# Optimization experiments

Measured on AMD Instinct MI355X. Metric: run time of the kernel, lower is better.

## Reference

```python
import jax, jax.numpy as jnp
import numpy as np

N_TOKENS = 16384  # bs*slen = 4*4096
HIDDEN = 2048
EXPERTS = 8
TOPK = 2
EPS = 1e-20


def setup_inputs() -> dict:
    key = jax.random.key(0)
    k1, k2, k3 = jax.random.split(key, 3)
    x = jax.random.normal(k1, (N_TOKENS, HIDDEN), dtype=jnp.float32)
    W = jax.random.normal(k2, (EXPERTS, HIDDEN), dtype=jnp.float32) * 0.02
    expert_bias = jax.random.normal(k3, (EXPERTS,), dtype=jnp.float32) * 0.01
    return {"x": x, "W": W, "expert_bias": expert_bias}


def reference(x, W, expert_bias):
    # gate: linear without bias -> (N, experts)
    logits = jnp.einsum("nd,ed->ne", x, W)
    scores = jax.nn.sigmoid(logits.astype(jnp.float32))
    # topk on biased scores, but gather unbiased scores
    _, selected_experts_indices = jax.lax.top_k(scores + expert_bias[None, :], TOPK)
    top_scores = jnp.take_along_axis(scores, selected_experts_indices, axis=1)
    # renormalize
    top_scores = top_scores / (top_scores.sum(axis=-1, keepdims=True) + EPS)
    # entropy on detached scores
    d = jax.lax.stop_gradient(top_scores)
    experts_entropy = -(d * jnp.log(d)).sum(axis=-1).mean()
    # histogram over expert indices (torch.histc with bins=E, min=0, max=E)
    num_tokens_per_expert = jnp.bincount(
        selected_experts_indices.reshape(-1), length=EXPERTS
    )
    return (top_scores, scores, selected_experts_indices,
            num_tokens_per_expert, experts_entropy)
```

## Files before the change

### kernel.cpp

```cpp
#include <hip/hip_runtime.h>
#include <math.h>

#define NT  16384
#define HID 2048
#define NE  8
#define NBLK 512

constexpr int TOP_OFF  = 0;
constexpr int SC_OFF   = NT * 2;
constexpr int IDX_OFF  = SC_OFF + NT * NE;
constexpr int HIST_OFF = IDX_OFF + NT * 2;
constexpr int ENT_OFF  = HIST_OFF + NE;

constexpr int WS_ROW = 12;

__global__ void init_tail(float* __restrict__ out) {
  const int i = threadIdx.x;
  if (i < NE + 1) out[HIST_OFF + i] = 0.0f;
}

#define FOR_E(F) F(0) F(1) F(2) F(3) F(4) F(5) F(6) F(7)

template <bool USE_WS>
__global__ __launch_bounds__(512, 4)
void router_kernel(const float* __restrict__ x, const float* __restrict__ W,
                   const float* __restrict__ bias, float* __restrict__ out,
                   float* __restrict__ ws) {
  __shared__ float sW[NE * HID];
  __shared__ int   sHist[NE];
  __shared__ float sEnt;

  const int tid  = threadIdx.x;
  const int wave = tid >> 6;
  const int lane = tid & 63;

  {
    const float4* Wv  = reinterpret_cast<const float4*>(W);
    float4*       sWv = reinterpret_cast<float4*>(sW);
#pragma unroll
    for (int i = 0; i < 8; ++i) sWv[i * 512 + tid] = Wv[i * 512 + tid];
  }
  if (tid < NE) sHist[tid] = 0;
  if (tid == 0) sEnt = 0.0f;

#define DECL_BS(e) const float bs_##e = bias[e];
  FOR_E(DECL_BS)

  __syncthreads();

  const int t0 = blockIdx.x * 32 + wave * 4;
  const float* xb = x + (size_t)t0 * HID;
  const int phase = (wave + (int)blockIdx.x) & 7;

#define DECL_ACC(e) float a0_##e = 0.f, a1_##e = 0.f, a2_##e = 0.f, a3_##e = 0.f;
  FOR_E(DECL_ACC)

#pragma unroll
  for (int it = 0; it < 8; ++it) {
    const int itr = (it + phase) & 7;
    const int off = itr * 256 + lane * 4;
    const float4 x0 = *reinterpret_cast<const float4*>(xb + off);
    const float4 x1 = *reinterpret_cast<const float4*>(xb + HID + off);
    const float4 x2 = *reinterpret_cast<const float4*>(xb + 2 * HID + off);
    const float4 x3 = *reinterpret_cast<const float4*>(xb + 3 * HID + off);
#define STEP_E(e)                                                          \
    {                                                                      \
      const float4 wv = *reinterpret_cast<const float4*>(sW + e * HID + off); \
      a0_##e += x0.x * wv.x + x0.y * wv.y + x0.z * wv.z + x0.w * wv.w;     \
      a1_##e += x1.x * wv.x + x1.y * wv.y + x1.z * wv.z + x1.w * wv.w;     \
      a2_##e += x2.x * wv.x + x2.y * wv.y + x2.z * wv.z + x2.w * wv.w;     \
      a3_##e += x3.x * wv.x + x3.y * wv.y + x3.z * wv.z + x3.w * wv.w;     \
    }
    FOR_E(STEP_E)
  }

#define RED(v)                                                             \
  { v += __shfl_xor(v, 32, 64); v += __shfl_xor(v, 16, 64);                \
    v += __shfl_xor(v,  8, 64); v += __shfl_xor(v,  4, 64);                \
    v += __shfl_xor(v,  2, 64); v += __shfl_xor(v,  1, 64); }
#define RED_E(e) RED(a0_##e) RED(a1_##e) RED(a2_##e) RED(a3_##e)
  FOR_E(RED_E)

#define SEL_E(e)                                                           \
  float le_##e = a0_##e;                                                   \
  le_##e = (lane == 1) ? a1_##e : le_##e;                                  \
  le_##e = (lane == 2) ? a2_##e : le_##e;                                  \
  le_##e = (lane == 3) ? a3_##e : le_##e;
  FOR_E(SEL_E)

  if (lane < 4) {
    const int tok = t0 + lane;
#define SIG_E(e) const float sc_##e = 1.0f / (1.0f + __expf(-le_##e));
    FOR_E(SIG_E)

    float m1 = -1e30f, m2 = -1e30f, s1 = 0.0f, s2 = 0.0f;
    int i1 = 0, i2 = 0;
#define TOP_E(e)                                                           \
    {                                                                      \
      const float be = sc_##e + bs_##e;                                    \
      const bool g1 = be > m1;                                             \
      const bool g2 = be > m2;                                             \
      i2 = g1 ? i1 : (g2 ? e     : i2);                                    \
      m2 = g1 ? m1 : (g2 ? be    : m2);                                    \
      s2 = g1 ? s1 : (g2 ? sc_##e : s2);                                   \
      i1 = g1 ? e     : i1;                                                \
      m1 = g1 ? be    : m1;                                                \
      s1 = g1 ? sc_##e : s1;                                               \
    }
    FOR_E(TOP_E)

    const float denom = s1 + s2 + 1e-20f;
    const float n1 = s1 / denom;
    const float n2 = s2 / denom;

    *reinterpret_cast<float2*>(out + TOP_OFF + (size_t)tok * 2) =
        make_float2(n1, n2);
    *reinterpret_cast<float2*>(out + IDX_OFF + (size_t)tok * 2) =
        make_float2((float)i1, (float)i2);
    *reinterpret_cast<float4*>(out + SC_OFF + (size_t)tok * 8) =
        make_float4(sc_0, sc_1, sc_2, sc_3);
    *reinterpret_cast<float4*>(out + SC_OFF + (size_t)tok * 8 + 4) =
        make_float4(sc_4, sc_5, sc_6, sc_7);

    const float ent = -(n1 * __logf(n1) + n2 * __logf(n2));
    atomicAdd(&sEnt, ent);
    atomicAdd(&sHist[i1], 1);
    atomicAdd(&sHist[i2], 1);
  }

  __syncthreads();
  if (USE_WS) {
    if (tid < NE) ws[(size_t)blockIdx.x * WS_ROW + tid] = (float)sHist[tid];
    if (tid == NE) ws[(size_t)blockIdx.x * WS_ROW + NE] = sEnt;
  } else {
    if (tid < NE) atomicAdd(out + HIST_OFF + tid, (float)sHist[tid]);
    if (tid == 0) atomicAdd(out + ENT_OFF, sEnt * (1.0f / (float)NT));
  }
}

__global__ void finalize(const float* __restrict__ ws, float* __restrict__ out) {
  const int lane = threadIdx.x & 63;
  float h0 = 0.f, h1 = 0.f, h2 = 0.f, h3 = 0.f;
  float h4 = 0.f, h5 = 0.f, h6 = 0.f, h7 = 0.f, ent = 0.f;
#pragma unroll
  for (int r = 0; r < NBLK / 64; ++r) {
    const float* p = ws + (size_t)(r * 64 + lane) * WS_ROW;
    h0 += p[0]; h1 += p[1]; h2 += p[2]; h3 += p[3];
    h4 += p[4]; h5 += p[5]; h6 += p[6]; h7 += p[7];
    ent += p[8];
  }
#define REDF(v)                                                            \
  { v += __shfl_xor(v, 32, 64); v += __shfl_xor(v, 16, 64);                \
    v += __shfl_xor(v,  8, 64); v += __shfl_xor(v,  4, 64);                \
    v += __shfl_xor(v,  2, 64); v += __shfl_xor(v,  1, 64); }
  REDF(h0) REDF(h1) REDF(h2) REDF(h3) REDF(h4) REDF(h5) REDF(h6) REDF(h7)
  REDF(ent)
  if (lane == 0) {
    out[HIST_OFF + 0] = h0; out[HIST_OFF + 1] = h1;
    out[HIST_OFF + 2] = h2; out[HIST_OFF + 3] = h3;
    out[HIST_OFF + 4] = h4; out[HIST_OFF + 5] = h5;
    out[HIST_OFF + 6] = h6; out[HIST_OFF + 7] = h7;
    out[ENT_OFF] = ent * (1.0f / (float)NT);
  }
}

extern "C" void kernel_launch(void* const* d_in, const int* in_sizes, int n_in,
                              void* d_out, int out_size, void* d_ws, size_t ws_size,
                              hipStream_t stream) {
  (void)in_sizes; (void)n_in; (void)out_size;
  const float* x    = (const float*)d_in[0];
  const float* W    = (const float*)d_in[1];
  const float* bias = (const float*)d_in[2];
  float* out = (float*)d_out;

  const bool use_ws = (d_ws != nullptr) &&
                      (ws_size >= (size_t)NBLK * WS_ROW * sizeof(float));
  if (use_ws) {
    router_kernel<true><<<NBLK, 512, 0, stream>>>(x, W, bias, out, (float*)d_ws);
    finalize<<<1, 64, 0, stream>>>((const float*)d_ws, out);
  } else {
    init_tail<<<1, 64, 0, stream>>>(out);
    router_kernel<false><<<NBLK, 512, 0, stream>>>(x, W, bias, out, (float*)d_ws);
  }
}
```

Measured before the change: 36.38 us.

## Prefetch first x chunk before W staging and use transpose-style butterfly reduction

Issues the first iteration's x loads before copying W into shared memory and waiting at the barrier, so global latency overlaps the LDS fill. It drops the per-wave phase rotation and uses a plain chunk order. It replaces 32 independent full butterfly reductions with a staged exchange that halves the shuffle count by trading values between lane halves, leaving each 16-lane group holding one token's logits. The entropy is then reduced across groups before a single shared atomic. Extra registers are held across the barrier, which may affect occupancy at launch bounds 512,4.

```diff
diff --git a/kernel.cpp b/kernel.cpp
--- a/kernel.cpp
+++ b/kernel.cpp
@@ -34,6 +34,15 @@
   const int wave = tid >> 6;
   const int lane = tid & 63;
 
+  const int t0 = blockIdx.x * 32 + wave * 4;
+  const float* xb = x + (size_t)t0 * HID;
+
+  const int off0 = lane * 4;
+  const float4 p0 = *reinterpret_cast<const float4*>(xb + off0);
+  const float4 p1 = *reinterpret_cast<const float4*>(xb + HID + off0);
+  const float4 p2 = *reinterpret_cast<const float4*>(xb + 2 * HID + off0);
+  const float4 p3 = *reinterpret_cast<const float4*>(xb + 3 * HID + off0);
+
   {
     const float4* Wv  = reinterpret_cast<const float4*>(W);
     float4*       sWv = reinterpret_cast<float4*>(sW);
@@ -48,17 +57,22 @@
 
   __syncthreads();
 
-  const int t0 = blockIdx.x * 32 + wave * 4;
-  const float* xb = x + (size_t)t0 * HID;
-  const int phase = (wave + (int)blockIdx.x) & 7;
-
 #define DECL_ACC(e) float a0_##e = 0.f, a1_##e = 0.f, a2_##e = 0.f, a3_##e = 0.f;
   FOR_E(DECL_ACC)
 
+#define STEP0_E(e)                                                         \
+  {                                                                        \
+    const float4 wv = *reinterpret_cast<const float4*>(sW + e * HID + off0); \
+    a0_##e += p0.x * wv.x + p0.y * wv.y + p0.z * wv.z + p0.w * wv.w;       \
+    a1_##e += p1.x * wv.x + p1.y * wv.y + p1.z * wv.z + p1.w * wv.w;       \
+    a2_##e += p2.x * wv.x + p2.y * wv.y + p2.z * wv.z + p2.w * wv.w;       \
+    a3_##e += p3.x * wv.x + p3.y * wv.y + p3.z * wv.z + p3.w * wv.w;       \
+  }
+  FOR_E(STEP0_E)
+
 #pragma unroll
-  for (int it = 0; it < 8; ++it) {
-    const int itr = (it + phase) & 7;
-    const int off = itr * 256 + lane * 4;
+  for (int it = 1; it < 8; ++it) {
+    const int off = it * 256 + lane * 4;
     const float4 x0 = *reinterpret_cast<const float4*>(xb + off);
     const float4 x1 = *reinterpret_cast<const float4*>(xb + HID + off);
     const float4 x2 = *reinterpret_cast<const float4*>(xb + 2 * HID + off);
@@ -74,45 +88,62 @@
     FOR_E(STEP_E)
   }
 
-#define RED(v)                                                             \
-  { v += __shfl_xor(v, 32, 64); v += __shfl_xor(v, 16, 64);                \
-    v += __shfl_xor(v,  8, 64); v += __shfl_xor(v,  4, 64);                \
-    v += __shfl_xor(v,  2, 64); v += __shfl_xor(v,  1, 64); }
-#define RED_E(e) RED(a0_##e) RED(a1_##e) RED(a2_##e) RED(a3_##e)
-  FOR_E(RED_E)
-
-#define SEL_E(e)                                                           \
-  float le_##e = a0_##e;                                                   \
-  le_##e = (lane == 1) ? a1_##e : le_##e;                                  \
-  le_##e = (lane == 2) ? a2_##e : le_##e;                                  \
-  le_##e = (lane == 3) ? a3_##e : le_##e;
-  FOR_E(SEL_E)
-
-  if (lane < 4) {
-    const int tok = t0 + lane;
-#define SIG_E(e) const float sc_##e = 1.0f / (1.0f + __expf(-le_##e));
-    FOR_E(SIG_E)
-
-    float m1 = -1e30f, m2 = -1e30f, s1 = 0.0f, s2 = 0.0f;
-    int i1 = 0, i2 = 0;
+  const bool lo  = (lane < 32);
+  const bool md  = ((lane & 16) == 0);
+#define STAGE_A(e)                                                         \
+  float b0_##e, b1_##e;                                                    \
+  {                                                                        \
+    float s0 = lo ? a2_##e : a0_##e;                                       \
+    float s1 = lo ? a3_##e : a1_##e;                                       \
+    const float r0 = __shfl_xor(s0, 32, 64);                               \
+    const float r1 = __shfl_xor(s1, 32, 64);                               \
+    b0_##e = (lo ? a0_##e : a2_##e) + r0;                                  \
+    b1_##e = (lo ? a1_##e : a3_##e) + r1;                                  \
+  }
+  FOR_E(STAGE_A)
+#define STAGE_B(e)                                                         \
+  float c_##e;                                                             \
+  {                                                                        \
+    float s = md ? b1_##e : b0_##e;                                        \
+    const float r = __shfl_xor(s, 16, 64);                                 \
+    c_##e = (md ? b0_##e : b1_##e) + r;                                    \
+  }
+  FOR_E(STAGE_B)
+#define STAGE_CF(e)                                                        \
+  c_##e += __shfl_xor(c_##e, 8, 64);                                       \
+  c_##e += __shfl_xor(c_##e, 4, 64);                                       \
+  c_##e += __shfl_xor(c_##e, 2, 64);                                       \
+  c_##e += __shfl_xor(c_##e, 1, 64);
+  FOR_E(STAGE_CF)
+
+  const int tok = t0 + (lane >> 4);
+#define SIG_E(e) const float sc_##e = 1.0f / (1.0f + __expf(-c_##e));
+  FOR_E(SIG_E)
+
+  float m1 = -1e30f, m2 = -1e30f, s1 = 0.0f, s2 = 0.0f;
+  int i1 = 0, i2 = 0;
 #define TOP_E(e)                                                           \
-    {                                                                      \
-      const float be = sc_##e + bs_##e;                                    \
-      const bool g1 = be > m1;                                             \
-      const bool g2 = be > m2;                                             \
-      i2 = g1 ? i1 : (g2 ? e     : i2);                                    \
-      m2 = g1 ? m1 : (g2 ? be    : m2);                                    \
-      s2 = g1 ? s1 : (g2 ? sc_##e : s2);                                   \
-      i1 = g1 ? e     : i1;                                                \
-      m1 = g1 ? be    : m1;                                                \
-      s1 = g1 ? sc_##e : s1;                                               \
-    }
-    FOR_E(TOP_E)
-
-    const float denom = s1 + s2 + 1e-20f;
-    const float n1 = s1 / denom;
-    const float n2 = s2 / denom;
-
+  {                                                                        \
+    const float be = sc_##e + bs_##e;                                      \
+    const bool g1 = be > m1;                                               \
+    const bool g2 = be > m2;                                               \
+    i2 = g1 ? i1 : (g2 ? e     : i2);                                      \
+    m2 = g1 ? m1 : (g2 ? be    : m2);                                      \
+    s2 = g1 ? s1 : (g2 ? sc_##e : s2);                                     \
+    i1 = g1 ? e     : i1;                                                  \
+    m1 = g1 ? be    : m1;                                                  \
+    s1 = g1 ? sc_##e : s1;                                                 \
+  }
+  FOR_E(TOP_E)
+
+  const float denom = s1 + s2 + 1e-20f;
+  const float n1 = s1 / denom;
+  const float n2 = s2 / denom;
+  float ent = -(n1 * __logf(n1) + n2 * __logf(n2));
+  float ent2 = ent + __shfl_xor(ent, 16, 64);
+  float ent4 = ent2 + __shfl_xor(ent2, 32, 64);
+
+  if ((lane & 15) == 0) {
     *reinterpret_cast<float2*>(out + TOP_OFF + (size_t)tok * 2) =
         make_float2(n1, n2);
     *reinterpret_cast<float2*>(out + IDX_OFF + (size_t)tok * 2) =
@@ -121,12 +152,10 @@
         make_float4(sc_0, sc_1, sc_2, sc_3);
     *reinterpret_cast<float4*>(out + SC_OFF + (size_t)tok * 8 + 4) =
         make_float4(sc_4, sc_5, sc_6, sc_7);
-
-    const float ent = -(n1 * __logf(n1) + n2 * __logf(n2));
-    atomicAdd(&sEnt, ent);
     atomicAdd(&sHist[i1], 1);
     atomicAdd(&sHist[i2], 1);
   }
+  if (lane == 0) atomicAdd(&sEnt, ent4);
 
   __syncthreads();
   if (USE_WS) {
```

After: 42.07 us. 15.6% more time.
